# Kernel optimization log

Measured on AMD Instinct MI355X. Metric: run time of the kernel, lower is better.

The kernel has to match this reference:

```python
import jax, jax.numpy as jnp
import numpy as np

N_AQI, N_MEO = 35, 18
N = N_AQI + N_MEO
F_OUT = 64
CTX = 60
D = F_OUT + CTX            # per-node feature dim inside pairwise concat
ALPHA = 0.2                # leakyrelu negative slope
B = 4096
IN_AQI, IN_MEO = 16, 16
NEG = -1e12


def _xavier(key, shape):
    fan_in, fan_out = shape[0], shape[-1]
    gain = 1.414
    bound = gain * np.sqrt(6.0 / (fan_in + fan_out))
    return jax.random.uniform(key, shape, jnp.float32, -bound, bound)


def setup_inputs() -> dict:
    key = jax.random.key(0)
    ks = jax.random.split(key, 32)
    inp = {
        "aqi_inp": jax.random.normal(ks[0], (B, N_AQI, IN_AQI), jnp.float32),
        "meo_inp": jax.random.normal(ks[1], (B, N_MEO, IN_MEO), jnp.float32),
        "context_feat": jax.random.normal(ks[2], (N, CTX), jnp.float32),
        "adj_norm": jax.random.uniform(ks[3], (N, N), jnp.float32),
        # embedding tables (all 2-dim embeddings as in the module)
        "aqi_idE": jax.random.normal(ks[4], (35, 2), jnp.float32),
        "aqi_monthE": jax.random.normal(ks[5], (13, 2), jnp.float32),
        "aqi_weekdayE": jax.random.normal(ks[6], (7, 2), jnp.float32),
        "aqi_hourE": jax.random.normal(ks[7], (24, 2), jnp.float32),
        "meo_windE": jax.random.normal(ks[8], (9, 2), jnp.float32),
        "meo_idE": jax.random.normal(ks[9], (18, 2), jnp.float32),
        "meo_monthE": jax.random.normal(ks[10], (13, 2), jnp.float32),
        "meo_weekdayE": jax.random.normal(ks[11], (7, 2), jnp.float32),
        "meo_hourE": jax.random.normal(ks[12], (24, 2), jnp.float32),
        # projection weights
        "W_xa": _xavier(ks[13], (IN_AQI, F_OUT)),
        "W_xm": _xavier(ks[14], (IN_MEO, F_OUT)),
        "W_ua": _xavier(ks[15], (IN_AQI + 8, F_OUT)),
        "W_um": _xavier(ks[16], (IN_MEO + 10, F_OUT)),
        # attention vectors: 2*F_OUT + 121 = 2*D + 1
        "a_aa": _xavier(ks[17], (2 * F_OUT + 121, 1)),
        "a_am": _xavier(ks[18], (2 * F_OUT + 121, 1)),
        "a_ma": _xavier(ks[19], (2 * F_OUT + 121, 1)),
        "a_mm": _xavier(ks[20], (2 * F_OUT + 121, 1)),
        # integer inputs
        "aqi_ex": jax.random.randint(ks[21], (B, N_AQI, 4), 0, 7, jnp.int32),
        "meo_ex": jax.random.randint(ks[22], (B, N_MEO, 5), 0, 7, jnp.int32),
        "adj": jax.random.randint(ks[23], (N, N), 0, 2, jnp.int32),
    }
    return inp


def _block(hf_src, hf_dst, an_block, a):
    # e[b,i,j] = leakyrelu(hf_src[b,i].a_src + hf_dst[b,j].a_dst + an[i,j]*a_last)
    d = hf_src.shape[-1]
    s = hf_src @ a[:d, 0]                        # [B, Ns]
    t = hf_dst @ a[d:2 * d, 0]                   # [B, Nd]
    e = s[:, :, None] + t[:, None, :] + an_block * a[2 * d, 0]
    return jax.nn.leaky_relu(e, ALPHA)


def reference(aqi_inp, meo_inp, context_feat, adj_norm,
              aqi_idE, aqi_monthE, aqi_weekdayE, aqi_hourE,
              meo_windE, meo_idE, meo_monthE, meo_weekdayE, meo_hourE,
              W_xa, W_xm, W_ua, W_um, a_aa, a_am, a_ma, a_mm,
              aqi_ex, meo_ex, adj):
    # value projection (pre-embedding features)
    attri_aqi = aqi_inp @ W_xa                   # [B, 35, F]
    attri_meo = meo_inp @ W_xm                   # [B, 18, F]
    heter_attri = jnp.concatenate([attri_aqi, attri_meo], axis=1)  # [B, 53, F]

    # append external-feature embeddings
    aqi_full = jnp.concatenate([
        aqi_inp, aqi_idE[aqi_ex[:, :, 0]], aqi_monthE[aqi_ex[:, :, 1]],
        aqi_weekdayE[aqi_ex[:, :, 2]], aqi_hourE[aqi_ex[:, :, 3]]], axis=2)
    meo_full = jnp.concatenate([
        meo_inp, meo_windE[meo_ex[:, :, 0]], meo_idE[meo_ex[:, :, 1]],
        meo_monthE[meo_ex[:, :, 2]], meo_weekdayE[meo_ex[:, :, 3]],
        meo_hourE[meo_ex[:, :, 4]]], axis=2)

    heter_aqi = aqi_full @ W_ua                  # [B, 35, F]
    heter_meo = meo_full @ W_um                  # [B, 18, F]
    hf = jnp.concatenate([heter_aqi, heter_meo], axis=1)            # [B, 53, F]
    ctx = jnp.broadcast_to(context_feat[None], (hf.shape[0], N, CTX))
    hf = jnp.concatenate([hf, ctx], axis=2)      # [B, 53, D]

    # pairwise scores per heterogeneous sub-block (decomposed, no N*N*D tensor)
    hfa, hfm = hf[:, :N_AQI], hf[:, N_AQI:]
    e_aa = _block(hfa, hfa, adj_norm[:N_AQI, :N_AQI], a_aa)
    e_am = _block(hfa, hfm, adj_norm[:N_AQI, N_AQI:], a_am)
    e_ma = _block(hfm, hfa, adj_norm[N_AQI:, :N_AQI], a_ma)
    e_mm = _block(hfm, hfm, adj_norm[N_AQI:, N_AQI:], a_mm)
    e = jnp.concatenate([
        jnp.concatenate([e_aa, e_am], axis=2),
        jnp.concatenate([e_ma, e_mm], axis=2)], axis=1)             # [B, 53, 53]

    attention = jax.nn.softmax(jnp.where(adj[None] > 0, e, NEG), axis=2)
    heter_out = attention @ heter_attri          # [B, 53, F]
    return heter_out[:, :N_AQI, :], heter_out[:, N_AQI:, :]
```

## Files before the change

kernel.cpp:

```cpp
#include <hip/hip_runtime.h>
#include <hip/hip_bf16.h>

#define NAQ 35
#define NME 18
#define NN  53
#define FD  64
#define CTXD 60
#define PERB 2

#define CVI_F   1024
#define CVE_F   1152
#define SVC_F   1248
#define EBW_F   1460
#define WS_FLOATS 4428

#define L_CVI   0
#define L_CVE   128
#define L_SVC   224
#define L_AF    436
#define L_EFA   1716
#define L_EFM   2031
#define L_SVW   2229
#define L_PT    2444
#define L_ATT   4748
#define S_TOTAL 7052
#define P_STR   72
#define AF_STR  40

typedef unsigned int   u32;
typedef unsigned short u16;
typedef short s8v __attribute__((ext_vector_type(8)));
typedef float f4v __attribute__((ext_vector_type(4)));

__device__ __forceinline__ float ldf(const void* p, long i, bool bf) {
  if (bf) { u16 h = ((const u16*)p)[i]; return __uint_as_float(((u32)h) << 16); }
  return ((const float*)p)[i];
}
__device__ __forceinline__ u16 f2bf(float f) {
  u32 u = __float_as_uint(f);
  return (u16)((u + 0x7FFFu + ((u >> 16) & 1u)) >> 16);
}
__device__ __forceinline__ bool sniff_bf16(const void* ctx) {
  const u32* w = (const u32*)ctx;
  bool ok = true;
#pragma unroll
  for (int k = 0; k < 32; ++k) {
    u32 e = (w[k] >> 7) & 0xFFu;
    ok = ok && (e >= 96u && e <= 160u);
  }
  return ok;
}
__device__ __forceinline__ s8v ld_frag(const u16* p) {
  union { float4 f; s8v s; } u;
  u.f = *(const float4*)(const void*)p;
  return u.s;
}

__global__ void prep_kernel(
    const void* __restrict__ ctx, const void* __restrict__ adjn,
    const void* __restrict__ Wxa, const void* __restrict__ Wxm,
    const void* __restrict__ Wua, const void* __restrict__ Wum,
    const void* __restrict__ a_aa, const void* __restrict__ a_am,
    const void* __restrict__ a_ma, const void* __restrict__ a_mm,
    const int* __restrict__ adj, float* __restrict__ ws)
{
  const bool bf = sniff_bf16(ctx);
  int tid = blockIdx.x * blockDim.x + threadIdx.x;
  if (tid < 2048) {
    int n = tid >> 5, kk = tid & 31;
    float v = (kk < 16) ? ldf(Wxa, kk * 64 + n, bf)
                        : ldf(Wxm, (kk - 16) * 64 + n, bf);
    ((u16*)ws)[tid] = f2bf(v);
    return;
  }
  int fi = tid - 1024;
  if (fi < CVE_F) {
    int idx = fi - CVI_F;
    int tr = idx >> 4, k = idx & 15;
    const void* Wu = (tr < 4) ? Wua : Wum;
    const void* av; int off;
    switch (tr) {
      case 0: av = a_aa; off = 0;   break;
      case 1: av = a_am; off = 0;   break;
      case 2: av = a_aa; off = 124; break;
      case 3: av = a_ma; off = 124; break;
      case 4: av = a_ma; off = 0;   break;
      case 5: av = a_mm; off = 0;   break;
      case 6: av = a_am; off = 124; break;
      default: av = a_mm; off = 124; break;
    }
    float s = 0.f;
    for (int f = 0; f < 64; ++f) s += ldf(Wu, k * 64 + f, bf) * ldf(av, off + f, bf);
    ws[fi] = s;
  } else if (fi < SVC_F) {
    int idx = fi - CVE_F;
    int tr = idx / 12, e = idx - tr * 12;
    int E = (tr < 4) ? 8 : 10;
    float v = 0.f;
    if (e < E) {
      const void* Wu = (tr < 4) ? Wua : Wum;
      const void* av; int off;
      switch (tr) {
        case 0: av = a_aa; off = 0;   break;
        case 1: av = a_am; off = 0;   break;
        case 2: av = a_aa; off = 124; break;
        case 3: av = a_ma; off = 124; break;
        case 4: av = a_ma; off = 0;   break;
        case 5: av = a_mm; off = 0;   break;
        case 6: av = a_am; off = 124; break;
        default: av = a_mm; off = 124; break;
      }
      float s = 0.f;
      for (int f = 0; f < 64; ++f) s += ldf(Wu, (16 + e) * 64 + f, bf) * ldf(av, off + f, bf);
      v = s;
    }
    ws[fi] = v;
  } else if (fi < EBW_F) {
    int idx = fi - SVC_F;
    int arr = idx / 53, i = idx - arr * 53;
    int isA = (i < NAQ);
    const void* av; int off;
    if (arr == 0)      { av = isA ? a_aa : a_ma; off = 64;  }
    else if (arr == 1) { av = isA ? a_am : a_mm; off = 64;  }
    else if (arr == 2) { av = isA ? a_aa : a_am; off = 188; }
    else               { av = isA ? a_ma : a_mm; off = 188; }
    float s = 0.f;
    for (int c = 0; c < CTXD; ++c) s += ldf(ctx, i * CTXD + c, bf) * ldf(av, off + c, bf);
    ws[fi] = s;
  } else if (fi < WS_FLOATS) {
    int idx = fi - EBW_F;
    int i = idx / 56, j = idx - i * 56;
    float v = 1e30f;
    if (j < NN && adj[i * NN + j] > 0) {
      const void* aq = (i < NAQ) ? ((j < NAQ) ? a_aa : a_am)
                                 : ((j < NAQ) ? a_ma : a_mm);
      v = ldf(adjn, i * NN + j, bf) * ldf(aq, 248, bf);
    }
    ws[fi] = v;
  }
}

__global__ __launch_bounds__(256, 5) void hga_main(
    const void* __restrict__ aqi_inp, const void* __restrict__ meo_inp,
    const void* __restrict__ ctx,
    const void* __restrict__ aqi_idE, const void* __restrict__ aqi_monthE,
    const void* __restrict__ aqi_weekdayE, const void* __restrict__ aqi_hourE,
    const void* __restrict__ meo_windE, const void* __restrict__ meo_idE,
    const void* __restrict__ meo_monthE, const void* __restrict__ meo_weekdayE,
    const void* __restrict__ meo_hourE,
    const int* __restrict__ aqi_ex, const int* __restrict__ meo_ex,
    const float* __restrict__ ws, void* __restrict__ out, int B)
{
  __shared__ __align__(16) float sm[S_TOTAL];
  const int t = threadIdx.x;
  const bool bf = sniff_bf16(ctx);
  u16* AFu = (u16*)(sm + L_AF);
  u16* ATu = (u16*)(sm + L_ATT);
  u16* Pu  = (u16*)(sm + L_PT);

  {
    const float4* src = (const float4*)(ws + CVI_F);
    float4* dst = (float4*)sm;
    for (int v = t; v < 109; v += 256) dst[v] = src[v];
  }
  __syncthreads();

  for (int e = 0; e < PERB; ++e) {
    const int b = blockIdx.x * PERB + e;
    if (b >= B) break;

    for (int idx = t; idx < 654; idx += 256) {
      if (idx < 140) {
        int r = idx >> 2, j = idx & 3;
        uint2 v;
        if (bf) v = ((const uint2*)aqi_inp)[((long)b * NAQ + r) * 4 + j];
        else {
          float4 f = ((const float4*)aqi_inp)[((long)b * NAQ + r) * 4 + j];
          v.x = ((u32)f2bf(f.y) << 16) | f2bf(f.x);
          v.y = ((u32)f2bf(f.w) << 16) | f2bf(f.z);
        }
        *(uint2*)(AFu + r * AF_STR + j * 4) = v;
      } else if (idx < 212) {
        int z = idx - 140;
        int i = z >> 2, j = z & 3;
        uint2 v;
        if (bf) v = ((const uint2*)meo_inp)[((long)b * NME + i) * 4 + j];
        else {
          float4 f = ((const float4*)meo_inp)[((long)b * NME + i) * 4 + j];
          v.x = ((u32)f2bf(f.y) << 16) | f2bf(f.x);
          v.y = ((u32)f2bf(f.w) << 16) | f2bf(f.z);
        }
        *(uint2*)(AFu + (NAQ + i) * AF_STR + 16 + j * 4) = v;
      } else if (idx < 352) {
        int z = idx - 212;
        int r = z >> 2, j = z & 3;
        *(uint2*)(AFu + r * AF_STR + 16 + j * 4) = make_uint2(0, 0);
      } else if (idx < 424) {
        int z = idx - 352;
        int i = z >> 2, j = z & 3;
        *(uint2*)(AFu + (NAQ + i) * AF_STR + j * 4) = make_uint2(0, 0);
      } else if (idx < 564) {
        int z = idx - 424;
        int r = z >> 2, p = z & 3;
        int ee = aqi_ex[((long)b * NAQ + r) * 4 + p];
        const void* tbl = (p == 0) ? aqi_idE : (p == 1) ? aqi_monthE
                         : (p == 2) ? aqi_weekdayE : aqi_hourE;
        sm[L_EFA + r * 9 + p * 2]     = ldf(tbl, ee * 2, bf);
        sm[L_EFA + r * 9 + p * 2 + 1] = ldf(tbl, ee * 2 + 1, bf);
      } else {
        int z = idx - 564;
        int i = z / 5, p = z - i * 5;
        int ee = meo_ex[((long)b * NME + i) * 5 + p];
        const void* tbl = (p == 0) ? meo_windE : (p == 1) ? meo_idE
                         : (p == 2) ? meo_monthE : (p == 3) ? meo_weekdayE : meo_hourE;
        sm[L_EFM + i * 11 + p * 2]     = ldf(tbl, ee * 2, bf);
        sm[L_EFM + i * 11 + p * 2 + 1] = ldf(tbl, ee * 2 + 1, bf);
      }
    }
    {
      int c = t & 63;
      for (int kk = t >> 6; kk < 11; kk += 4) ATu[c * P_STR + 53 + kk] = 0;
    }
    __syncthreads();

    {
      const int lane = t & 63, w = t >> 6;
      const int mm = lane & 15, q4 = lane >> 4;
      s8v av = ld_frag(AFu + (16 * w + mm) * AF_STR + q4 * 8);
      const u16* wt = (const u16*)ws;
      s8v bv0 = ld_frag(wt + (mm)      * 32 + q4 * 8);
      s8v bv1 = ld_frag(wt + (16 + mm) * 32 + q4 * 8);
      s8v bv2 = ld_frag(wt + (32 + mm) * 32 + q4 * 8);
      s8v bv3 = ld_frag(wt + (48 + mm) * 32 + q4 * 8);
#pragma unroll
      for (int nt = 0; nt < 4; ++nt) {
        f4v acc = {0.f, 0.f, 0.f, 0.f};
        s8v bv = (nt == 0) ? bv0 : (nt == 1) ? bv1 : (nt == 2) ? bv2 : bv3;
        acc = __builtin_amdgcn_mfma_f32_16x16x32_bf16(av, bv, acc, 0, 0, 0);
        const int c = nt * 16 + mm;
#pragma unroll
        for (int reg = 0; reg < 4; ++reg) {
          const int r = 16 * w + q4 * 4 + reg;
          if (r < NN) ATu[c * P_STR + r] = f2bf(acc[reg]);
        }
      }
      if (t < 212) {
        const int r = t >> 2, role = t & 3;
        const bool isA = (r < NAQ);
        const int tr = (isA ? 0 : 4) + role;
        const u16* arow = AFu + r * AF_STR + (isA ? 0 : 16);
        const float* Ci = sm + L_CVI + tr * 16;
        float s = 0.f;
#pragma unroll
        for (int k = 0; k < 16; ++k)
          s = fmaf(__uint_as_float(((u32)arow[k]) << 16), Ci[k], s);
        const int E = isA ? 8 : 10;
        const float* Ef = isA ? (sm + L_EFA + r * 9) : (sm + L_EFM + (r - NAQ) * 11);
        const float* Ce = sm + L_CVE + tr * 12;
        for (int k = 0; k < E; ++k) s = fmaf(Ef[k], Ce[k], s);
        sm[L_SVW + role * 53 + r] = sm[L_SVC + role * 53 + r] + s;
      }
    }
    __syncthreads();

    {
      const int r = t >> 2, q = t & 3;
      const int j0 = q * 14;
      if (r < NN) {
        float ev[14];
        float m = -3.0e38f, ssum = 0.f;
        const float s1 = sm[L_SVW + r], s2 = sm[L_SVW + 53 + r];
        const float* tb = sm + L_SVW + ((r < NAQ) ? 106 : 159);
        const float* ebrow = ws + EBW_F + r * 56;
#pragma unroll
        for (int jj = 0; jj < 14; ++jj) {
          const int j = j0 + jj;
          float v = -3.0e38f;
          if (j < NN) {
            float eb = ebrow[j];
            float rr = ((j < NAQ) ? s1 : s2) + tb[j] + eb;
            v = (eb > 1e29f) ? -1.0e12f : ((rr > 0.f) ? rr : 0.2f * rr);
          }
          ev[jj] = v;
          m = fmaxf(m, v);
        }
        m = fmaxf(m, __shfl_xor(m, 1, 64));
        m = fmaxf(m, __shfl_xor(m, 2, 64));
#pragma unroll
        for (int jj = 0; jj < 14; ++jj) {
          float pv = ((j0 + jj) < NN) ? __expf(ev[jj] - m) : 0.f;
          ev[jj] = pv;
          ssum += pv;
        }
        ssum += __shfl_xor(ssum, 1, 64);
        ssum += __shfl_xor(ssum, 2, 64);
        const float rinv = 1.f / ssum;
#pragma unroll
        for (int jj = 0; jj < 14; ++jj) {
          const int j = j0 + jj;
          Pu[r * P_STR + j] = (j < NN) ? f2bf(ev[jj] * rinv) : (u16)0;
        }
        if (q == 0) *(uint4*)(Pu + r * P_STR + 56) = make_uint4(0, 0, 0, 0);
      } else {
        for (int idx = t - 212; idx < 99; idx += 44) {
          int row = 53 + idx / 9, o = idx - (idx / 9) * 9;
          *(uint4*)(Pu + row * P_STR + o * 8) = make_uint4(0, 0, 0, 0);
        }
      }
    }
    __syncthreads();

    {
      const int lane = t & 63, w = t >> 6;
      const int mm = lane & 15, q4 = lane >> 4;
      const u16* Ar = Pu + (16 * w + mm) * P_STR + q4 * 8;
      s8v av0 = ld_frag(Ar);
      s8v av1 = ld_frag(Ar + 32);
#pragma unroll
      for (int nt = 0; nt < 4; ++nt) {
        const u16* Br = ATu + (16 * nt + mm) * P_STR + q4 * 8;
        s8v bv0 = ld_frag(Br);
        s8v bv1 = ld_frag(Br + 32);
        f4v acc = {0.f, 0.f, 0.f, 0.f};
        acc = __builtin_amdgcn_mfma_f32_16x16x32_bf16(av0, bv0, acc, 0, 0, 0);
        acc = __builtin_amdgcn_mfma_f32_16x16x32_bf16(av1, bv1, acc, 0, 0, 0);
        const int cgl = 16 * nt + mm;
#pragma unroll
        for (int reg = 0; reg < 4; ++reg) {
          const int rg = 16 * w + q4 * 4 + reg;
          if (rg < NN) {
            long off = (rg < NAQ)
              ? (long)b * (NAQ * FD) + (long)rg * FD + cgl
              : (long)B * (NAQ * FD) + (long)b * (NME * FD) + (long)(rg - NAQ) * FD + cgl;
            if (bf) ((u16*)out)[off] = f2bf(acc[reg]);
            else    ((float*)out)[off] = acc[reg];
          }
        }
      }
    }
    __syncthreads();
  }
}

extern "C" void kernel_launch(void* const* d_in, const int* in_sizes, int n_in,
                              void* d_out, int out_size, void* d_ws, size_t ws_size,
                              hipStream_t stream)
{
  const void* aqi_inp      = d_in[0];
  const void* meo_inp      = d_in[1];
  const void* ctx          = d_in[2];
  const void* adjn         = d_in[3];
  const void* aqi_idE      = d_in[4];
  const void* aqi_monthE   = d_in[5];
  const void* aqi_weekdayE = d_in[6];
  const void* aqi_hourE    = d_in[7];
  const void* meo_windE    = d_in[8];
  const void* meo_idE      = d_in[9];
  const void* meo_monthE   = d_in[10];
  const void* meo_weekdayE = d_in[11];
  const void* meo_hourE    = d_in[12];
  const void* Wxa          = d_in[13];
  const void* Wxm          = d_in[14];
  const void* Wua          = d_in[15];
  const void* Wum          = d_in[16];
  const void* a_aa         = d_in[17];
  const void* a_am         = d_in[18];
  const void* a_ma         = d_in[19];
  const void* a_mm         = d_in[20];
  const int*  aqi_ex       = (const int*)d_in[21];
  const int*  meo_ex       = (const int*)d_in[22];
  const int*  adj          = (const int*)d_in[23];
  float* ws = (float*)d_ws;
  const int B = in_sizes[0] / (NAQ * 16);

  hipLaunchKernelGGL(prep_kernel, dim3((5452 + 255) / 256), dim3(256), 0, stream,
                     ctx, adjn, Wxa, Wxm, Wua, Wum, a_aa, a_am, a_ma, a_mm, adj, ws);
  hipLaunchKernelGGL(hga_main, dim3((B + PERB - 1) / PERB), dim3(256), 0, stream,
                     aqi_inp, meo_inp, ctx, aqi_idE, aqi_monthE, aqi_weekdayE, aqi_hourE,
                     meo_windE, meo_idE, meo_monthE, meo_weekdayE, meo_hourE,
                     aqi_ex, meo_ex, ws, d_out, B);
}
```

Baseline: 178.9 us.

## Cache embedding tables in LDS, hoist weight frags, stage output through LDS

Embedding tables are copied into shared memory once per block, so per-element gathers read LDS instead of global memory. The weight fragments are loaded once before the batch loop rather than once per batch element. The final output is staged through LDS as bf16 and written with vectorised row stores. The LDS layout is overlapped to shrink shared memory, and launch bounds are raised to allow more resident blocks. In fp32 mode the output is now rounded through bf16 before being stored, and the extra barriers and staging pass add work per element.

```diff
diff --git a/kernel.cpp b/kernel.cpp
--- a/kernel.cpp
+++ b/kernel.cpp
@@ -17,13 +17,14 @@
 #define L_CVI   0
 #define L_CVE   128
 #define L_SVC   224
-#define L_AF    436
-#define L_EFA   1716
-#define L_EFM   2031
-#define L_SVW   2229
-#define L_PT    2444
-#define L_ATT   4748
-#define S_TOTAL 7052
+#define L_ETA   436
+#define L_AF    736
+#define L_EFA   2016
+#define L_EFM   2331
+#define L_PT    736
+#define L_ATT   3040
+#define L_SVW   5344
+#define S_TOTAL 5556
 #define P_STR   72
 #define AF_STR  40
 
@@ -140,7 +141,7 @@
   }
 }
 
-__global__ __launch_bounds__(256, 5) void hga_main(
+__global__ __launch_bounds__(256, 7) void hga_main(
     const void* __restrict__ aqi_inp, const void* __restrict__ meo_inp,
     const void* __restrict__ ctx,
     const void* __restrict__ aqi_idE, const void* __restrict__ aqi_monthE,
@@ -162,7 +163,27 @@
     const float4* src = (const float4*)(ws + CVI_F);
     float4* dst = (float4*)sm;
     for (int v = t; v < 109; v += 256) dst[v] = src[v];
+    for (int i = t; i < 300; i += 256) {
+      const void* srcp; int off;
+      if (i < 70)       { srcp = aqi_idE;      off = i;       }
+      else if (i < 96)  { srcp = aqi_monthE;   off = i - 70;  }
+      else if (i < 110) { srcp = aqi_weekdayE; off = i - 96;  }
+      else if (i < 158) { srcp = aqi_hourE;    off = i - 110; }
+      else if (i < 176) { srcp = meo_windE;    off = i - 158; }
+      else if (i < 212) { srcp = meo_idE;      off = i - 176; }
+      else if (i < 238) { srcp = meo_monthE;   off = i - 212; }
+      else if (i < 252) { srcp = meo_weekdayE; off = i - 238; }
+      else              { srcp = meo_hourE;    off = i - 252; }
+      sm[L_ETA + i] = ldf(srcp, off, bf);
+    }
   }
+  const int lane = t & 63, w = t >> 6;
+  const int mm = lane & 15, q4 = lane >> 4;
+  const u16* wt = (const u16*)ws;
+  s8v wb0 = ld_frag(wt + (mm)      * 32 + q4 * 8);
+  s8v wb1 = ld_frag(wt + (16 + mm) * 32 + q4 * 8);
+  s8v wb2 = ld_frag(wt + (32 + mm) * 32 + q4 * 8);
+  s8v wb3 = ld_frag(wt + (48 + mm) * 32 + q4 * 8);
   __syncthreads();
 
   for (int e = 0; e < PERB; ++e) {
@@ -203,18 +224,17 @@
         int z = idx - 424;
         int r = z >> 2, p = z & 3;
         int ee = aqi_ex[((long)b * NAQ + r) * 4 + p];
-        const void* tbl = (p == 0) ? aqi_idE : (p == 1) ? aqi_monthE
-                         : (p == 2) ? aqi_weekdayE : aqi_hourE;
-        sm[L_EFA + r * 9 + p * 2]     = ldf(tbl, ee * 2, bf);
-        sm[L_EFA + r * 9 + p * 2 + 1] = ldf(tbl, ee * 2 + 1, bf);
+        int base = L_ETA + ((p == 0) ? 0 : (p == 1) ? 70 : (p == 2) ? 96 : 110);
+        sm[L_EFA + r * 9 + p * 2]     = sm[base + ee * 2];
+        sm[L_EFA + r * 9 + p * 2 + 1] = sm[base + ee * 2 + 1];
       } else {
         int z = idx - 564;
         int i = z / 5, p = z - i * 5;
         int ee = meo_ex[((long)b * NME + i) * 5 + p];
-        const void* tbl = (p == 0) ? meo_windE : (p == 1) ? meo_idE
-                         : (p == 2) ? meo_monthE : (p == 3) ? meo_weekdayE : meo_hourE;
-        sm[L_EFM + i * 11 + p * 2]     = ldf(tbl, ee * 2, bf);
-        sm[L_EFM + i * 11 + p * 2 + 1] = ldf(tbl, ee * 2 + 1, bf);
+        int base = L_ETA + 158 + ((p == 0) ? 0 : (p == 1) ? 18 : (p == 2) ? 54
+                                 : (p == 3) ? 80 : 94);
+        sm[L_EFM + i * 11 + p * 2]     = sm[base + ee * 2];
+        sm[L_EFM + i * 11 + p * 2 + 1] = sm[base + ee * 2 + 1];
       }
     }
     {
@@ -224,18 +244,11 @@
     __syncthreads();
 
     {
-      const int lane = t & 63, w = t >> 6;
-      const int mm = lane & 15, q4 = lane >> 4;
       s8v av = ld_frag(AFu + (16 * w + mm) * AF_STR + q4 * 8);
-      const u16* wt = (const u16*)ws;
-      s8v bv0 = ld_frag(wt + (mm)      * 32 + q4 * 8);
-      s8v bv1 = ld_frag(wt + (16 + mm) * 32 + q4 * 8);
-      s8v bv2 = ld_frag(wt + (32 + mm) * 32 + q4 * 8);
-      s8v bv3 = ld_frag(wt + (48 + mm) * 32 + q4 * 8);
 #pragma unroll
       for (int nt = 0; nt < 4; ++nt) {
         f4v acc = {0.f, 0.f, 0.f, 0.f};
-        s8v bv = (nt == 0) ? bv0 : (nt == 1) ? bv1 : (nt == 2) ? bv2 : bv3;
+        s8v bv = (nt == 0) ? wb0 : (nt == 1) ? wb1 : (nt == 2) ? wb2 : wb3;
         acc = __builtin_amdgcn_mfma_f32_16x16x32_bf16(av, bv, acc, 0, 0, 0);
         const int c = nt * 16 + mm;
 #pragma unroll
@@ -311,31 +324,47 @@
     __syncthreads();
 
     {
-      const int lane = t & 63, w = t >> 6;
-      const int mm = lane & 15, q4 = lane >> 4;
       const u16* Ar = Pu + (16 * w + mm) * P_STR + q4 * 8;
       s8v av0 = ld_frag(Ar);
       s8v av1 = ld_frag(Ar + 32);
+      f4v acc[4];
 #pragma unroll
       for (int nt = 0; nt < 4; ++nt) {
         const u16* Br = ATu + (16 * nt + mm) * P_STR + q4 * 8;
         s8v bv0 = ld_frag(Br);
         s8v bv1 = ld_frag(Br + 32);
-        f4v acc = {0.f, 0.f, 0.f, 0.f};
-        acc = __builtin_amdgcn_mfma_f32_16x16x32_bf16(av0, bv0, acc, 0, 0, 0);
-        acc = __builtin_amdgcn_mfma_f32_16x16x32_bf16(av1, bv1, acc, 0, 0, 0);
+        f4v a = {0.f, 0.f, 0.f, 0.f};
+        a = __builtin_amdgcn_mfma_f32_16x16x32_bf16(av0, bv0, a, 0, 0, 0);
+        a = __builtin_amdgcn_mfma_f32_16x16x32_bf16(av1, bv1, a, 0, 0, 0);
+        acc[nt] = a;
+      }
+      __syncthreads();
+#pragma unroll
+      for (int nt = 0; nt < 4; ++nt) {
         const int cgl = 16 * nt + mm;
 #pragma unroll
         for (int reg = 0; reg < 4; ++reg) {
           const int rg = 16 * w + q4 * 4 + reg;
-          if (rg < NN) {
-            long off = (rg < NAQ)
-              ? (long)b * (NAQ * FD) + (long)rg * FD + cgl
-              : (long)B * (NAQ * FD) + (long)b * (NME * FD) + (long)(rg - NAQ) * FD + cgl;
-            if (bf) ((u16*)out)[off] = f2bf(acc[reg]);
-            else    ((float*)out)[off] = acc[reg];
-          }
-        }
+          if (rg < NN) Pu[rg * P_STR + cgl] = f2bf(acc[nt][reg]);
+        }
+      }
+    }
+    __syncthreads();
+
+    for (int idx = t; idx < 424; idx += 256) {
+      int r = idx >> 3, o = idx & 7;
+      long off = (r < NAQ)
+        ? (long)b * (NAQ * FD) + (long)r * FD + o * 8
+        : (long)B * (NAQ * FD) + (long)b * (NME * FD) + (long)(r - NAQ) * FD + o * 8;
+      uint4 v = *(const uint4*)(Pu + r * P_STR + o * 8);
+      if (bf) {
+        *(uint4*)((u16*)out + off) = v;
+      } else {
+        float* po = (float*)out + off;
+        po[0] = __uint_as_float(v.x << 16); po[1] = __uint_as_float(v.x & 0xFFFF0000u);
+        po[2] = __uint_as_float(v.y << 16); po[3] = __uint_as_float(v.y & 0xFFFF0000u);
+        po[4] = __uint_as_float(v.z << 16); po[5] = __uint_as_float(v.z & 0xFFFF0000u);
+        po[6] = __uint_as_float(v.w << 16); po[7] = __uint_as_float(v.w & 0xFFFF0000u);
       }
     }
     __syncthreads();
```

After: 206.2 us. +15.3%, slower.
